# Performance work log

Measured on AMD Instinct MI355X. Metric: run time of the kernel, lower is better.

Reference implementation:

```python
import jax, jax.numpy as jnp
import numpy as np

BSZ, SLEN, DIN = 4, 2048, 1024
EMB, HNO = 1024, 16
HSZ = EMB // HNO


def setup_inputs() -> dict:
    key = jax.random.key(0)
    ks = jax.random.split(key, 7)
    s = 1.0 / np.sqrt(DIN)
    return {
        "x": jax.random.normal(ks[0], (BSZ, SLEN, DIN), dtype=jnp.float32),
        "Wq": jax.random.uniform(ks[1], (EMB, DIN), jnp.float32, -s, s),
        "bq": jax.random.uniform(ks[2], (EMB,), jnp.float32, -s, s),
        "Wk": jax.random.uniform(ks[3], (EMB, DIN), jnp.float32, -s, s),
        "bk": jax.random.uniform(ks[4], (EMB,), jnp.float32, -s, s),
        "Wv": jax.random.uniform(ks[5], (EMB, DIN), jnp.float32, -s, s),
        "bv": jax.random.uniform(ks[6], (EMB,), jnp.float32, -s, s),
    }


def reference(x, Wq, bq, Wk, bk, Wv, bv):
    bsz, slen, _ = x.shape
    # QKV projections, split heads: [b, h, s, hd]
    def proj(W, b):
        y = jnp.einsum('bsd,ed->bse', x, W) + b
        return y.reshape(bsz, slen, HNO, HSZ).transpose(0, 2, 1, 3)
    q, k, v = proj(Wq, bq), proj(Wk, bk), proj(Wv, bv)
    # scaled causal attention scores [b, h, s, s]
    scores = jnp.einsum('bhqd,bhkd->bhqk', q, k) / jnp.sqrt(jnp.asarray(HSZ, x.dtype))
    causal = jnp.tril(jnp.ones((slen, slen), dtype=bool))
    scores = jnp.where(causal[None, None], scores, -jnp.inf)
    attn = jax.nn.softmax(scores, axis=-1)
    value = jnp.einsum('bhqk,bhkd->bhqd', attn, v)  # [b, h, s, hd]
    # faithful to source: swap (s, hd) THEN flatten to [b, s, emb]
    value = jnp.swapaxes(value, -2, -1).reshape(bsz, slen, -1)
    return value
```

## Files before the change

kernel.cpp:

```cpp
#include <hip/hip_runtime.h>


#define BSZ 4
#define SLEN 2048
#define DIN 1024
#define EMB 1024
#define HNO 16
#define HSZ 64

typedef unsigned short u16;
typedef __bf16 bf16x8_t __attribute__((ext_vector_type(8)));
typedef float f32x4_t __attribute__((ext_vector_type(4)));

__device__ __forceinline__ u16 f2bf(float f) {
    unsigned u = __float_as_uint(f);
    u += 0x7FFFu + ((u >> 16) & 1u);
    return (u16)(u >> 16);
}

__device__ __forceinline__ float exp2_fast(float x) {
    float r;
    asm("v_exp_f32 %0, %1" : "=v"(r) : "v"(x));
    return r;
}

__device__ __forceinline__ unsigned cvt_pk_bf16(float lo, float hi) {
    unsigned r;
    asm("v_cvt_pk_bf16_f32 %0, %1, %2" : "=v"(r) : "v"(lo), "v"(hi));
    return r;
}

__device__ __forceinline__ void gld16(void* lds, const void* g) {
    __builtin_amdgcn_global_load_lds(
        (const __attribute__((address_space(1))) void*)g,
        (__attribute__((address_space(3))) void*)lds, 16, 0, 0);
}

__global__ __launch_bounds__(256) void cvt_bf16_kernel(
    const float* __restrict__ x,  const float* __restrict__ wq,
    const float* __restrict__ wk, const float* __restrict__ wv,
    u16* __restrict__ xo, u16* __restrict__ wo)
{
    const int y = blockIdx.y;
    const float* src = (y == 0) ? x : (y == 1) ? wq : (y == 2) ? wk : wv;
    u16* dst = (y == 0) ? xo : wo + (size_t)(y - 1) * (EMB * DIN);
    const int n8 = (y == 0) ? (BSZ * SLEN * DIN / 8) : (EMB * DIN / 8);

    for (int i = blockIdx.x * 256 + threadIdx.x; i < n8; i += gridDim.x * 256) {
        float4 a = *reinterpret_cast<const float4*>(src + (size_t)i * 8);
        float4 b = *reinterpret_cast<const float4*>(src + (size_t)i * 8 + 4);
        union { u16 h[8]; uint4 u; } p;
        p.h[0] = f2bf(a.x); p.h[1] = f2bf(a.y); p.h[2] = f2bf(a.z); p.h[3] = f2bf(a.w);
        p.h[4] = f2bf(b.x); p.h[5] = f2bf(b.y); p.h[6] = f2bf(b.z); p.h[7] = f2bf(b.w);
        *reinterpret_cast<uint4*>(dst + (size_t)i * 8) = p.u;
    }
}

#define FENCE() asm volatile("" ::: "memory")

#define RD_A4(mb, kk, buf)                                                     \
    _Pragma("unroll")                                                          \
    for (int mm = 0; mm < 4; ++mm)                                             \
        af[mm][kk] = *reinterpret_cast<const bf16x8_t*>(                       \
            AsF + (buf) * 16384 + aBase + ((mb) + mm) * 1024 +                 \
            ((kk) ? (s0 ^ 32) : s0));

#define RD_B3(kk, buf)                                                         \
    _Pragma("unroll")                                                          \
    for (int nn = 0; nn < 3; ++nn)                                             \
        bf[nn][kk] = *reinterpret_cast<const bf16x8_t*>(                       \
            BsF + (buf) * 12288 + bBase + nn * 1024 +                          \
            ((kk) ? (s0 ^ 32) : s0));

#define STAGE_A(buf, kt, u)                                                    \
    gld16(AsF + (buf) * 16384 + (u) * 4096 + t * 8,                            \
          srcA + (size_t)(u) * 64 * DIN + (kt) * 64)

#define STAGE_B(buf, kt, u)                                                    \
    gld16(BsF + (buf) * 12288 + (u) * 4096 + t * 8,                            \
          srcB + (size_t)(u) * 64 * DIN + (kt) * 64)

#define BAR_LGKM()                                                             \
    __builtin_amdgcn_s_barrier();                                              \
    asm volatile("s_waitcnt lgkmcnt(0)" ::: "memory");                         \
    __builtin_amdgcn_sched_barrier(0);                                         \
    __builtin_amdgcn_s_setprio(1)

#define MFMA12(mb, kk)                                                         \
    _Pragma("unroll")                                                          \
    for (int mm = 0; mm < 4; ++mm) {                                           \
        _Pragma("unroll")                                                      \
        for (int nn = 0; nn < 3; ++nn)                                         \
            acc[(mb) + mm][nn] = __builtin_amdgcn_mfma_f32_16x16x32_bf16(      \
                af[mm][kk], bf[nn][kk], acc[(mb) + mm][nn], 0, 0, 0);          \
    }

#define MFMA_END()                                                             \
    __builtin_amdgcn_s_setprio(0);                                             \
    __builtin_amdgcn_sched_barrier(0)

__global__ __launch_bounds__(512, 2) void qkv_gemm_kernel(
    const u16* __restrict__ xb, const u16* __restrict__ wb,
    const float* __restrict__ bq, const float* __restrict__ bk,
    const float* __restrict__ bv, u16* __restrict__ qkv)
{
    __shared__ __attribute__((aligned(16))) u16 AsF[2 * 256 * 64];
    __shared__ __attribute__((aligned(16))) u16 BsF[2 * 192 * 64];

    const int t    = threadIdx.x;
    const int wid  = t >> 6;
    const int lane = t & 63;
    const int g    = lane >> 4;
    const int r16  = lane & 15;
    const int r8   = r16 & 7;
    const int wm   = wid >> 2;
    const int wn   = wid & 3;

    const int wg  = blockIdx.x;
    const int idx = (wg & 7) * 64 + (wg >> 3);
    const int bx  = idx >> 4;
    const int byn = idx & 15;
    const int m0  = bx * 256;
    const int n0g = byn * 192;

    const int rowoff = t >> 3;
    const int colswz = ((t & 7) ^ (rowoff & 7)) * 8;
    const u16* srcA = xb + (size_t)(m0 + rowoff) * DIN + colswz;
    const u16* srcB = wb + (size_t)(n0g + rowoff) * DIN + colswz;

    const int aBase = (wm * 128 + r16) * 64;
    const int bBase = (wn * 48 + r16) * 64;
    const int s0    = (g ^ r8) * 8;

    f32x4_t  acc[8][3] = {};
    bf16x8_t af[4][2], bf[3][2];

    STAGE_A(0, 0, 0); STAGE_A(0, 0, 1); STAGE_A(0, 0, 2); STAGE_A(0, 0, 3);
    STAGE_B(0, 0, 0); STAGE_B(0, 0, 1); STAGE_B(0, 0, 2);
    STAGE_B(1, 1, 0); STAGE_B(1, 1, 1); STAGE_B(1, 1, 2); STAGE_A(1, 1, 0);
    asm volatile("s_waitcnt vmcnt(4)" ::: "memory");
    __builtin_amdgcn_s_barrier();

#pragma unroll 1
    for (int i = 0; i < 8; ++i) {
        const bool last = (i == 7);
        const int  tb = 2 * i + 1;
        const int  ta = 2 * i + 2;
        const int  tc = 2 * i + 3;

        FENCE();
        RD_A4(0, 0, 0); RD_B3(0, 0);
        STAGE_A(1, tb, 2);
        BAR_LGKM(); MFMA12(0, 0); MFMA_END();
        __builtin_amdgcn_s_barrier();

        FENCE();
        RD_A4(0, 1, 0); RD_B3(1, 0);
        STAGE_A(1, tb, 1); STAGE_A(1, tb, 3);
        BAR_LGKM(); MFMA12(0, 1); MFMA_END();
        __builtin_amdgcn_s_barrier();

        FENCE();
        RD_A4(4, 0, 0);
        if (!last) { STAGE_B(0, ta, 0); STAGE_B(0, ta, 1); }
        BAR_LGKM(); MFMA12(4, 0); MFMA_END();
        __builtin_amdgcn_s_barrier();

        FENCE();
        RD_A4(4, 1, 0);
        if (!last) { STAGE_B(0, ta, 2); STAGE_A(0, ta, 0); }
        BAR_LGKM(); MFMA12(4, 1); MFMA_END();
        if (!last) asm volatile("s_waitcnt vmcnt(4)" ::: "memory");
        else       asm volatile("s_waitcnt vmcnt(0)" ::: "memory");
        __builtin_amdgcn_s_barrier();

        FENCE();
        RD_A4(0, 0, 1); RD_B3(0, 1);
        if (!last) STAGE_A(0, ta, 2);
        BAR_LGKM(); MFMA12(0, 0); MFMA_END();
        __builtin_amdgcn_s_barrier();

        FENCE();
        RD_A4(0, 1, 1); RD_B3(1, 1);
        if (!last) { STAGE_A(0, ta, 1); STAGE_A(0, ta, 3); }
        BAR_LGKM(); MFMA12(0, 1); MFMA_END();
        __builtin_amdgcn_s_barrier();

        FENCE();
        RD_A4(4, 0, 1);
        if (!last) { STAGE_B(1, tc, 0); STAGE_B(1, tc, 1); }
        BAR_LGKM(); MFMA12(4, 0); MFMA_END();
        __builtin_amdgcn_s_barrier();

        FENCE();
        RD_A4(4, 1, 1);
        if (!last) { STAGE_B(1, tc, 2); STAGE_A(1, tc, 0); }
        BAR_LGKM(); MFMA12(4, 1); MFMA_END();
        if (!last) asm volatile("s_waitcnt vmcnt(4)" ::: "memory");
        __builtin_amdgcn_s_barrier();
    }

    const size_t per = (size_t)BSZ * HNO * SLEN * HSZ;
#pragma unroll
    for (int nn = 0; nn < 3; ++nn) {
        const int egl = n0g + wn * 48 + nn * 16 + r16;
        const int mat = egl >> 10;
        const int e   = egl & 1023;
        const float* bp = (mat == 0) ? bq : (mat == 1) ? bk : bv;
        const float bval = bp[e];
        const float qsv  = (mat == 0) ? 0.125f * 1.44269504f : 1.0f;
        const int h = e >> 6, d = e & 63;
        u16* ob = qkv + (size_t)mat * per + (size_t)h * (SLEN * HSZ) + d;
#pragma unroll
        for (int mm = 0; mm < 8; ++mm) {
#pragma unroll
            for (int r = 0; r < 4; ++r) {
                int m = m0 + wm * 128 + mm * 16 + g * 4 + r;
                int b = m >> 11, s = m & 2047;
                ob[(size_t)b * (HNO * SLEN * HSZ) + (size_t)s * HSZ] =
                    f2bf((acc[mm][nn][r] + bval) * qsv);
            }
        }
    }
}

__global__ __launch_bounds__(512, 6) void attn_kernel(
    const u16* __restrict__ qb, const u16* __restrict__ kb,
    const u16* __restrict__ vb, float* __restrict__ out)
{
    __shared__ __attribute__((aligned(16))) u16 Ks[64][64];
    __shared__ __attribute__((aligned(16))) u16 Vt[64][72];
    __shared__ __attribute__((aligned(16))) u16 P2[8][16][72];

    const int t    = threadIdx.x;
    const int wid  = t >> 6;
    const int lane = t & 63;
    const int g    = lane >> 4;
    const int r16  = lane & 15;

    const int w   = blockIdx.x;
    const int idx = w >> 3;
    const int bh  = (w & 7) * 8 + (idx & 7);
    const int qt  = 15 - (idx >> 3);
    const int q0  = qt * 128;
    const size_t base = (size_t)bh * (SLEN * HSZ);

    const int qi = q0 + wid * 16 + r16;
    bf16x8_t qf0 = *reinterpret_cast<const bf16x8_t*>(&qb[base + (size_t)qi * HSZ + g * 8]);
    bf16x8_t qf1 = *reinterpret_cast<const bf16x8_t*>(&qb[base + (size_t)qi * HSZ + 32 + g * 8]);

    const int krl    = lane >> 3;
    const int kchunk = ((lane & 7) ^ krl) * 8;
    const int krow_g = wid * 8 + krl;
    u16* kdst = &Ks[wid * 8][0];

    const int va  = t & 31;
    const int vc4 = (t >> 5) * 4;

    const int ksl = ((g ^ (r16 & 7)) * 8);

    f32x4_t o[4] = {};
    float mrow = -1e30f, lrow = 0.f;

    const int ntiles = 2 * qt + 2;
    const int qw0 = q0 + wid * 16;
    const int qmax_wave = qw0 + 15;

    uint2 v0 = *reinterpret_cast<const uint2*>(&vb[base + (size_t)(2 * va) * HSZ + vc4]);
    uint2 v1 = *reinterpret_cast<const uint2*>(&vb[base + (size_t)(2 * va + 1) * HSZ + vc4]);

    for (int kt = 0; kt < ntiles; ++kt) {
        const int kv0 = kt * 64;
        __syncthreads();
        gld16(kdst, &kb[base + (size_t)(kv0 + krow_g) * HSZ + kchunk]);
        {
            const unsigned* pa = reinterpret_cast<const unsigned*>(&v0);
            const unsigned* pb = reinterpret_cast<const unsigned*>(&v1);
#pragma unroll
            for (int j2 = 0; j2 < 2; ++j2) {
                unsigned lo = __builtin_amdgcn_perm(pb[j2], pa[j2], 0x05040100u);
                unsigned hi = __builtin_amdgcn_perm(pb[j2], pa[j2], 0x07060302u);
                *reinterpret_cast<unsigned*>(&Vt[vc4 + 2 * j2][2 * va])     = lo;
                *reinterpret_cast<unsigned*>(&Vt[vc4 + 2 * j2 + 1][2 * va]) = hi;
            }
        }
        __syncthreads();

        if (kt + 1 < ntiles) {
            const size_t nb = base + (size_t)(kv0 + 64) * HSZ;
            v0 = *reinterpret_cast<const uint2*>(&vb[nb + (size_t)(2 * va) * HSZ + vc4]);
            v1 = *reinterpret_cast<const uint2*>(&vb[nb + (size_t)(2 * va + 1) * HSZ + vc4]);
        }

        if (kv0 > qmax_wave) continue;

        f32x4_t c_[4];
        __builtin_amdgcn_s_setprio(1);
#pragma unroll
        for (int m = 0; m < 4; ++m) {
            bf16x8_t a0 = *reinterpret_cast<const bf16x8_t*>(&Ks[m * 16 + r16][ksl]);
            bf16x8_t a1 = *reinterpret_cast<const bf16x8_t*>(&Ks[m * 16 + r16][ksl ^ 32]);
            f32x4_t cc = {};
            cc = __builtin_amdgcn_mfma_f32_16x16x32_bf16(a0, qf0, cc, 0, 0, 0);
            cc = __builtin_amdgcn_mfma_f32_16x16x32_bf16(a1, qf1, cc, 0, 0, 0);
            c_[m] = cc;
        }
        __builtin_amdgcn_s_setprio(0);

        float s[16];
        if (kv0 + 63 > qw0) {
#pragma unroll
            for (int m = 0; m < 4; ++m)
#pragma unroll
                for (int r = 0; r < 4; ++r) {
                    int kj = kv0 + m * 16 + g * 4 + r;
                    s[m * 4 + r] = (kj <= qi) ? c_[m][r] : -1e30f;
                }
        } else {
#pragma unroll
            for (int m = 0; m < 4; ++m)
#pragma unroll
                for (int r = 0; r < 4; ++r)
                    s[m * 4 + r] = c_[m][r];
        }
        float x0 = fmaxf(s[0], s[1]),   x1 = fmaxf(s[2], s[3]);
        float x2 = fmaxf(s[4], s[5]),   x3 = fmaxf(s[6], s[7]);
        float x4 = fmaxf(s[8], s[9]),   x5 = fmaxf(s[10], s[11]);
        float x6 = fmaxf(s[12], s[13]), x7 = fmaxf(s[14], s[15]);
        x0 = fmaxf(x0, x1); x2 = fmaxf(x2, x3); x4 = fmaxf(x4, x5); x6 = fmaxf(x6, x7);
        float tmax = fmaxf(fmaxf(x0, x2), fmaxf(x4, x6));
        tmax = fmaxf(tmax, __shfl_xor(tmax, 16));
        tmax = fmaxf(tmax, __shfl_xor(tmax, 32));

        if (!__all(tmax - mrow <= 8.0f)) {
            float mnew  = fmaxf(mrow, tmax);
            float alpha = exp2_fast(mrow - mnew);
#pragma unroll
            for (int j = 0; j < 4; ++j) {
                o[j][0] *= alpha; o[j][1] *= alpha; o[j][2] *= alpha; o[j][3] *= alpha;
            }
            lrow *= alpha;
            mrow = mnew;
        }

#pragma unroll
        for (int i = 0; i < 16; ++i)
            s[i] = exp2_fast(s[i] - mrow);
        float y0 = (s[0] + s[1]) + (s[2] + s[3]);
        float y1 = (s[4] + s[5]) + (s[6] + s[7]);
        float y2 = (s[8] + s[9]) + (s[10] + s[11]);
        float y3 = (s[12] + s[13]) + (s[14] + s[15]);
        float tsum = (y0 + y1) + (y2 + y3);
        tsum += __shfl_xor(tsum, 16);
        tsum += __shfl_xor(tsum, 32);
        lrow += tsum;

#pragma unroll
        for (int m = 0; m < 4; ++m) {
            uint2 pk;
            pk.x = cvt_pk_bf16(s[m * 4 + 0], s[m * 4 + 1]);
            pk.y = cvt_pk_bf16(s[m * 4 + 2], s[m * 4 + 3]);
            *reinterpret_cast<uint2*>(&P2[wid][r16][m * 16 + g * 4]) = pk;
        }

        __builtin_amdgcn_s_setprio(1);
#pragma unroll
        for (int c = 0; c < 2; ++c) {
            bf16x8_t pf = *reinterpret_cast<const bf16x8_t*>(&P2[wid][r16][c * 32 + g * 8]);
#pragma unroll
            for (int j = 0; j < 4; ++j) {
                bf16x8_t vf = *reinterpret_cast<const bf16x8_t*>(&Vt[j * 16 + r16][c * 32 + g * 8]);
                o[j] = __builtin_amdgcn_mfma_f32_16x16x32_bf16(vf, pf, o[j], 0, 0, 0);
            }
        }
        __builtin_amdgcn_s_setprio(0);
    }

    float rinv = 1.0f / lrow;
    const int b = bh >> 4, h = bh & 15;
    float* outb = out + (size_t)b * (SLEN * EMB) + (size_t)h * (HSZ * SLEN);
#pragma unroll
    for (int j = 0; j < 4; ++j) {
#pragma unroll
        for (int r = 0; r < 4; ++r) {
            int d = j * 16 + g * 4 + r;
            outb[(size_t)d * SLEN + qi] = o[j][r] * rinv;
        }
    }
}

extern "C" void kernel_launch(void* const* d_in, const int* in_sizes, int n_in,
                              void* d_out, int out_size, void* d_ws, size_t ws_size,
                              hipStream_t stream) {
    const float* x  = (const float*)d_in[0];
    const float* Wq = (const float*)d_in[1];
    const float* bq = (const float*)d_in[2];
    const float* Wk = (const float*)d_in[3];
    const float* bk = (const float*)d_in[4];
    const float* Wv = (const float*)d_in[5];
    const float* bv = (const float*)d_in[6];
    float* out = (float*)d_out;

    const size_t per = (size_t)BSZ * HNO * SLEN * HSZ;
    u16* qw = (u16*)d_ws;
    u16* kw = qw + per;
    u16* vw = kw + per;

    u16* xb = (u16*)d_out;
    u16* wb = xb + (size_t)BSZ * SLEN * DIN;

    cvt_bf16_kernel<<<dim3(256, 4), 256, 0, stream>>>(x, Wq, Wk, Wv, xb, wb);
    qkv_gemm_kernel<<<512, 512, 0, stream>>>(xb, wb, bq, bk, bv, qw);
    attn_kernel<<<1024, 512, 0, stream>>>(qw, kw, vw, out);
}
```

Baseline: 140.9 us.

## Rebalance QKV GEMM prefetch schedule, remap tile order, stage epilogue through LDS

Reorders the global-to-LDS staging in the QKV projection GEMM main loop so loads for the next tile are issued earlier. Waits become explicit vmcnt(7) checkpoints with scheduling barriers. Block-to-tile mapping is changed to a different grouping of M and N tiles, intended to improve L2 reuse. The epilogue now writes bias-added bf16 results into shared memory (padded rows) and then emits coalesced 16-byte global stores, replacing scattered 2-byte stores. This costs an extra LDS round trip and a block barrier.

```diff
diff --git a/kernel.cpp b/kernel.cpp
--- a/kernel.cpp
+++ b/kernel.cpp
@@ -99,13 +99,20 @@
     __builtin_amdgcn_s_setprio(0);                                             \
     __builtin_amdgcn_sched_barrier(0)
 
+#define VMW(n)                                                                 \
+    do {                                                                       \
+        asm volatile("s_waitcnt vmcnt(" #n ")" ::: "memory");                  \
+        __builtin_amdgcn_sched_barrier(0);                                     \
+    } while (0)
+
 __global__ __launch_bounds__(512, 2) void qkv_gemm_kernel(
     const u16* __restrict__ xb, const u16* __restrict__ wb,
     const float* __restrict__ bq, const float* __restrict__ bk,
     const float* __restrict__ bv, u16* __restrict__ qkv)
 {
-    __shared__ __attribute__((aligned(16))) u16 AsF[2 * 256 * 64];
-    __shared__ __attribute__((aligned(16))) u16 BsF[2 * 192 * 64];
+    __shared__ __attribute__((aligned(16))) u16 SH[2 * 256 * 64 + 2 * 192 * 64];
+    u16* AsF = SH;
+    u16* BsF = SH + 2 * 256 * 64;
 
     const int t    = threadIdx.x;
     const int wid  = t >> 6;
@@ -116,10 +123,11 @@
     const int wm   = wid >> 2;
     const int wn   = wid & 3;
 
-    const int wg  = blockIdx.x;
-    const int idx = (wg & 7) * 64 + (wg >> 3);
-    const int bx  = idx >> 4;
-    const int byn = idx & 15;
+    const int wg = blockIdx.x;
+    const int x  = wg & 7;
+    const int j  = wg >> 3;
+    const int bx  = (x >> 1) * 8 + (j >> 3);
+    const int byn = (x & 1) * 8 + (j & 7);
     const int m0  = bx * 256;
     const int n0g = byn * 192;
 
@@ -135,92 +143,106 @@
     f32x4_t  acc[8][3] = {};
     bf16x8_t af[4][2], bf[3][2];
 
-    STAGE_A(0, 0, 0); STAGE_A(0, 0, 1); STAGE_A(0, 0, 2); STAGE_A(0, 0, 3);
-    STAGE_B(0, 0, 0); STAGE_B(0, 0, 1); STAGE_B(0, 0, 2);
-    STAGE_B(1, 1, 0); STAGE_B(1, 1, 1); STAGE_B(1, 1, 2); STAGE_A(1, 1, 0);
-    asm volatile("s_waitcnt vmcnt(4)" ::: "memory");
+    STAGE_A(0, 0, 2); STAGE_B(0, 0, 0); STAGE_B(0, 0, 1); STAGE_B(0, 0, 2);
+    STAGE_A(0, 0, 0);
+    STAGE_A(0, 0, 1); STAGE_A(0, 0, 3);
+    STAGE_A(1, 1, 2); STAGE_B(1, 1, 0); STAGE_B(1, 1, 1); STAGE_B(1, 1, 2);
+    STAGE_A(1, 1, 0);
+    VMW(7);
     __builtin_amdgcn_s_barrier();
 
 #pragma unroll 1
     for (int i = 0; i < 8; ++i) {
-        const bool last = (i == 7);
-        const int  tb = 2 * i + 1;
+        const bool nl = (i != 7);
+        const int  tc = 2 * i + 1;
         const int  ta = 2 * i + 2;
-        const int  tc = 2 * i + 3;
+        const int  tn = 2 * i + 3;
 
         FENCE();
         RD_A4(0, 0, 0); RD_B3(0, 0);
-        STAGE_A(1, tb, 2);
         BAR_LGKM(); MFMA12(0, 0); MFMA_END();
         __builtin_amdgcn_s_barrier();
 
         FENCE();
         RD_A4(0, 1, 0); RD_B3(1, 0);
-        STAGE_A(1, tb, 1); STAGE_A(1, tb, 3);
+        STAGE_A(1, tc, 1); STAGE_A(1, tc, 3);
         BAR_LGKM(); MFMA12(0, 1); MFMA_END();
+        VMW(7);
         __builtin_amdgcn_s_barrier();
 
         FENCE();
         RD_A4(4, 0, 0);
-        if (!last) { STAGE_B(0, ta, 0); STAGE_B(0, ta, 1); }
+        if (nl) { STAGE_A(0, ta, 2); STAGE_B(0, ta, 0); }
         BAR_LGKM(); MFMA12(4, 0); MFMA_END();
         __builtin_amdgcn_s_barrier();
 
         FENCE();
         RD_A4(4, 1, 0);
-        if (!last) { STAGE_B(0, ta, 2); STAGE_A(0, ta, 0); }
+        if (nl) { STAGE_B(0, ta, 1); STAGE_B(0, ta, 2); STAGE_A(0, ta, 0); }
         BAR_LGKM(); MFMA12(4, 1); MFMA_END();
-        if (!last) asm volatile("s_waitcnt vmcnt(4)" ::: "memory");
-        else       asm volatile("s_waitcnt vmcnt(0)" ::: "memory");
+        if (nl) VMW(7); else VMW(2);
         __builtin_amdgcn_s_barrier();
 
         FENCE();
         RD_A4(0, 0, 1); RD_B3(0, 1);
-        if (!last) STAGE_A(0, ta, 2);
         BAR_LGKM(); MFMA12(0, 0); MFMA_END();
         __builtin_amdgcn_s_barrier();
 
         FENCE();
         RD_A4(0, 1, 1); RD_B3(1, 1);
-        if (!last) { STAGE_A(0, ta, 1); STAGE_A(0, ta, 3); }
+        if (nl) { STAGE_A(0, ta, 1); STAGE_A(0, ta, 3); }
         BAR_LGKM(); MFMA12(0, 1); MFMA_END();
+        if (nl) VMW(7); else VMW(0);
         __builtin_amdgcn_s_barrier();
 
         FENCE();
         RD_A4(4, 0, 1);
-        if (!last) { STAGE_B(1, tc, 0); STAGE_B(1, tc, 1); }
+        if (nl) { STAGE_A(1, tn, 2); STAGE_B(1, tn, 0); }
         BAR_LGKM(); MFMA12(4, 0); MFMA_END();
         __builtin_amdgcn_s_barrier();
 
         FENCE();
         RD_A4(4, 1, 1);
-        if (!last) { STAGE_B(1, tc, 2); STAGE_A(1, tc, 0); }
+        if (nl) { STAGE_B(1, tn, 1); STAGE_B(1, tn, 2); STAGE_A(1, tn, 0); }
         BAR_LGKM(); MFMA12(4, 1); MFMA_END();
-        if (!last) asm volatile("s_waitcnt vmcnt(4)" ::: "memory");
-        __builtin_amdgcn_s_barrier();
-    }
-
-    const size_t per = (size_t)BSZ * HNO * SLEN * HSZ;
+        if (nl) VMW(7);
+        __builtin_amdgcn_s_barrier();
+    }
+
+    u16* lout = SH;
 #pragma unroll
     for (int nn = 0; nn < 3; ++nn) {
-        const int egl = n0g + wn * 48 + nn * 16 + r16;
+        const int el  = wn * 48 + nn * 16 + r16;
+        const int egl = n0g + el;
         const int mat = egl >> 10;
         const int e   = egl & 1023;
         const float* bp = (mat == 0) ? bq : (mat == 1) ? bk : bv;
         const float bval = bp[e];
         const float qsv  = (mat == 0) ? 0.125f * 1.44269504f : 1.0f;
-        const int h = e >> 6, d = e & 63;
-        u16* ob = qkv + (size_t)mat * per + (size_t)h * (SLEN * HSZ) + d;
-#pragma unroll
-        for (int mm = 0; mm < 8; ++mm) {
+#pragma unroll
+        for (int mm = 0; mm < 8; ++mm)
 #pragma unroll
             for (int r = 0; r < 4; ++r) {
-                int m = m0 + wm * 128 + mm * 16 + g * 4 + r;
-                int b = m >> 11, s = m & 2047;
-                ob[(size_t)b * (HNO * SLEN * HSZ) + (size_t)s * HSZ] =
-                    f2bf((acc[mm][nn][r] + bval) * qsv);
+                int ml = wm * 128 + mm * 16 + g * 4 + r;
+                lout[ml * 196 + el] = f2bf((acc[mm][nn][r] + bval) * qsv);
             }
-        }
+    }
+    __syncthreads();
+
+    const size_t per = (size_t)BSZ * HNO * SLEN * HSZ;
+#pragma unroll
+    for (int it = 0; it < 12; ++it) {
+        int cid = it * 512 + t;
+        int row = cid / 24;
+        int cc  = cid - row * 24;
+        int egl = n0g + cc * 8;
+        int mat = egl >> 10;
+        int e   = egl & 1023;
+        int m   = m0 + row;
+        int b   = m >> 11, s = m & 2047;
+        uint4 v = *reinterpret_cast<const uint4*>(&lout[row * 196 + cc * 8]);
+        *reinterpret_cast<uint4*>(qkv + (size_t)mat * per +
+            ((((size_t)b * HNO) + (e >> 6)) * SLEN + s) * HSZ + (e & 63)) = v;
     }
 }
 
```

Result: faster. 130.5 us (-7.4%).
